# Optimization experiments

Measured on AMD Instinct MI355X. Metric: run time of the kernel, lower is better.

The kernel has to match this reference:

```python
import jax, jax.numpy as jnp
import numpy as np

DT = 0.1
WHEELBASE = 2.8
STATE_DIM = 12


def setup_inputs() -> dict:
    key = jax.random.key(0)
    k1, k2, k3 = jax.random.split(key, 3)
    b, l, h = 512, 64, 80
    x0 = jax.random.normal(k1, (b, STATE_DIM), dtype=jnp.float32)
    controls = jax.random.normal(k2, (b, l, h, 3), dtype=jnp.float32)
    deg = jax.random.uniform(k3, (b, 5), dtype=jnp.float32)
    return {"x0": x0, "controls": controls, "deg": deg}


def reference(x0, controls, deg):
    b, l, h, _ = controls.shape
    # degradation scales, broadcast over the l (candidate) dim: [b, 1]
    steer_scale = jnp.maximum(deg[:, 0:1], 0.05)
    brake_scale = jnp.maximum(deg[:, 1:2], 0.05)
    throttle_scale = jnp.maximum(deg[:, 2:3], 0.05)
    friction = jnp.maximum(deg[:, 4:5], 0.1)

    x_init = jnp.broadcast_to(x0[:, None, :], (b, l, x0.shape[-1]))  # [b,l,12]

    def step(x, u):  # x: [b,l,12], u: [b,l,3]
        delta = steer_scale * jnp.tanh(u[..., 0])
        fb = brake_scale * jax.nn.sigmoid(u[..., 1])
        fx = throttle_scale * jax.nn.sigmoid(u[..., 2])
        px, py, psi, vx, vy = (x[..., 0], x[..., 1], x[..., 2], x[..., 3], x[..., 4])
        speed = jnp.sqrt(vx * vx + vy * vy + 1e-06)
        acc = jnp.minimum(jnp.maximum(2.8 * fx - 6.5 * fb, -7.5 * friction), 3.0)
        speed2 = jnp.maximum(speed + acc * DT, 0.0)
        tan_d = jnp.tan(jnp.clip(delta, -0.75, 0.75))
        raw_yaw = speed2 / WHEELBASE * tan_d
        yaw_lim = jnp.maximum(friction * 9.81 / jnp.maximum(speed2, 2.0), 0.15)
        yaw_rate = jnp.clip(raw_yaw, -1.0, 1.0) * yaw_lim
        beta = jnp.clip(jnp.arctan(0.45 * tan_d), -0.65, 0.65)
        psi2 = psi + yaw_rate * DT
        vx2 = speed2 * jnp.cos(psi2 + beta)
        vy2 = speed2 * jnp.sin(psi2 + beta)
        px2 = px + vx2 * DT
        py2 = py + vy2 * DT
        ax = (vx2 - vx) / DT
        ay = (vy2 - vy) / DT
        x2 = jnp.stack([px2, py2, psi2, vx2, vy2, yaw_rate, ax, ay, beta, delta, fb, fx], -1)
        return x2, x2

    controls_t = jnp.moveaxis(controls, 2, 0)  # [h,b,l,3]
    _, traj = jax.lax.scan(step, x_init, controls_t)  # traj: [h,b,l,12]
    traj = jnp.concatenate([x_init[None], traj], axis=0)  # [h+1,b,l,12]
    return jnp.moveaxis(traj, 0, 2)  # [b,l,h+1,12]
```

## Files before the change

kernel.cpp:

```cpp
#include <hip/hip_runtime.h>
#include <math.h>


#define N_B 512
#define N_L 64
#define N_H 80
#define DT_F 0.1f
#define PITCH_F4 25
#define SPC 8
#define NCH 10

__device__ __forceinline__ float fast_rcp(float x) { return __builtin_amdgcn_rcpf(x); }

__device__ __forceinline__ float fast_tanh(float x) {
    const float e2 = __expf(2.0f * x);
    return (e2 - 1.0f) * fast_rcp(e2 + 1.0f);
}

__device__ __forceinline__ float fast_sigmoid(float x) {
    return fast_rcp(1.0f + __expf(-x));
}

__device__ __forceinline__ float fast_atan_small(float z) {
    const float z2 = z * z;
    float p = 1.0f / 9.0f;
    p = fmaf(p, z2, -1.0f / 7.0f);
    p = fmaf(p, z2, 1.0f / 5.0f);
    p = fmaf(p, z2, -1.0f / 3.0f);
    p = fmaf(p, z2, 1.0f);
    return z * p;
}

struct Ctl { float delta, fb, fx, tan_d, beta, acc; };

__device__ __forceinline__ Ctl make_ctl(float u0, float u1, float u2,
                                        float steer_scale, float brake_scale,
                                        float throttle_scale, float neg_brake_lim) {
    Ctl t;
    t.delta = steer_scale * fast_tanh(u0);
    t.fb = brake_scale    * fast_sigmoid(u1);
    t.fx = throttle_scale * fast_sigmoid(u2);
    const float dc = fminf(fmaxf(t.delta, -0.75f), 0.75f);
    float sd, cd;
    __sincosf(dc, &sd, &cd);
    t.tan_d = sd * fast_rcp(cd);
    t.beta = fminf(fmaxf(fast_atan_small(0.45f * t.tan_d), -0.65f), 0.65f);
    t.acc = fminf(fmaxf(2.8f * t.fx - 6.5f * t.fb, neg_brake_lim), 3.0f);
    return t;
}

__global__ __launch_bounds__(64) void degraded_bicycle_rollout_kernel(
    const float* __restrict__ x0,
    const float* __restrict__ controls,
    const float* __restrict__ deg,
    float* __restrict__ out)
{
    __shared__ float4 lds4[2][N_L * PITCH_F4];

    const int lane = threadIdx.x;
    const int b = blockIdx.x;
    const int tid = b * 64 + lane;

    const float* dg = deg + b * 5;
    const float steer_scale    = fmaxf(dg[0], 0.05f);
    const float brake_scale    = fmaxf(dg[1], 0.05f);
    const float throttle_scale = fmaxf(dg[2], 0.05f);
    const float friction       = fmaxf(dg[4], 0.1f);

    const float4* x0v = reinterpret_cast<const float4*>(x0 + b * 12);
    const float4 xi0 = x0v[0];
    const float4 xi1 = x0v[1];
    const float4 xi2 = x0v[2];

    {
        float4* ov = reinterpret_cast<float4*>(out + (size_t)tid * 972);
        ov[0] = xi0; ov[1] = xi1; ov[2] = xi2;
    }

    float px  = xi0.x;
    float py  = xi0.y;
    float psi = xi0.z;
    float vx  = xi0.w;
    float vy  = xi1.x;

    const float4* uc = reinterpret_cast<const float4*>(controls + (size_t)tid * 240);

    const float neg_brake_lim = -7.5f * friction;
    const float yaw_num = friction * 9.81f;
    const float inv_wheelbase = 1.0f / 2.8f;

    const size_t out_b = (size_t)b * 62208 + 12;

#define FLUSH_SLICE(FBUF, FC, I0, I1)                                             \
    {                                                                             \
        const size_t obase = out_b + (size_t)(FC) * (SPC * 12);                   \
        _Pragma("unroll")                                                         \
        for (int i = (I0); i < (I1); ++i) {                                       \
            const unsigned flat = i * 64 + lane;                                  \
            const unsigned l = flat / 24u;                                        \
            const unsigned q = flat - l * 24u;                                    \
            const float4 v = lds4[FBUF][l * PITCH_F4 + q];                        \
            *reinterpret_cast<float4*>(out + obase + (size_t)l * 972 + q * 4) = v;\
        }                                                                         \
    }

    float4 c0 = uc[0];
    float4 c1 = uc[1];
    float4 c2 = uc[2];

    for (int c = 0; c < NCH; ++c) {
        const int cur = c & 1;
        float4* lrow = &lds4[cur][lane * PITCH_F4];

        #pragma unroll
        for (int gg = 0; gg < 2; ++gg) {
            const int g = c * 2 + gg;
            float4 n0 = c0, n1 = c1, n2 = c2;
            if (g < 19) {
                n0 = uc[(g + 1) * 3 + 0];
                n1 = uc[(g + 1) * 3 + 1];
                n2 = uc[(g + 1) * 3 + 2];
            }

            const Ctl tA = make_ctl(c0.x, c0.y, c0.z, steer_scale, brake_scale, throttle_scale, neg_brake_lim);
            const Ctl tB = make_ctl(c0.w, c1.x, c1.y, steer_scale, brake_scale, throttle_scale, neg_brake_lim);
            const Ctl tC = make_ctl(c1.z, c1.w, c2.x, steer_scale, brake_scale, throttle_scale, neg_brake_lim);
            const Ctl tD = make_ctl(c2.y, c2.z, c2.w, steer_scale, brake_scale, throttle_scale, neg_brake_lim);

#define ROLL_STEP(T, RR)                                                          \
            {                                                                     \
                const float speed  = __builtin_amdgcn_sqrtf(fmaf(vx, vx, fmaf(vy, vy, 1e-6f))); \
                const float speed2 = fmaxf(fmaf((T).acc, DT_F, speed), 0.0f);     \
                const float raw_yaw = speed2 * inv_wheelbase * (T).tan_d;         \
                const float yaw_lim = fmaxf(yaw_num * fast_rcp(fmaxf(speed2, 2.0f)), 0.15f); \
                const float yaw_rate = fminf(fmaxf(raw_yaw, -1.0f), 1.0f) * yaw_lim; \
                const float psi2 = fmaf(yaw_rate, DT_F, psi);                     \
                float s_, c_;                                                     \
                __sincosf(psi2 + (T).beta, &s_, &c_);                             \
                const float vx2 = speed2 * c_;                                    \
                const float vy2 = speed2 * s_;                                    \
                const float px2 = fmaf(vx2, DT_F, px);                            \
                const float py2 = fmaf(vy2, DT_F, py);                            \
                const float ax = (vx2 - vx) * 10.0f;                              \
                const float ay = (vy2 - vy) * 10.0f;                              \
                lrow[(RR) * 3 + 0] = make_float4(px2, py2, psi2, vx2);            \
                lrow[(RR) * 3 + 1] = make_float4(vy2, yaw_rate, ax, ay);          \
                lrow[(RR) * 3 + 2] = make_float4((T).beta, (T).delta, (T).fb, (T).fx); \
                px = px2; py = py2; psi = psi2; vx = vx2; vy = vy2;               \
            }

            ROLL_STEP(tA, gg * 4 + 0)
            ROLL_STEP(tB, gg * 4 + 1)
            ROLL_STEP(tC, gg * 4 + 2)
            ROLL_STEP(tD, gg * 4 + 3)
#undef ROLL_STEP

            c0 = n0; c1 = n1; c2 = n2;

            if (c > 0) {
                if (gg == 0) FLUSH_SLICE(cur ^ 1, c - 1, 0, 12)
                else         FLUSH_SLICE(cur ^ 1, c - 1, 12, 24)
            }
        }
    }

    FLUSH_SLICE((NCH - 1) & 1, NCH - 1, 0, 24)
#undef FLUSH_SLICE
}

extern "C" void kernel_launch(void* const* d_in, const int* in_sizes, int n_in,
                              void* d_out, int out_size, void* d_ws, size_t ws_size,
                              hipStream_t stream) {
    (void)in_sizes; (void)n_in; (void)d_ws; (void)ws_size; (void)out_size;
    const float* x0       = (const float*)d_in[0];
    const float* controls = (const float*)d_in[1];
    const float* deg      = (const float*)d_in[2];
    float* out            = (float*)d_out;

    dim3 grid(N_B), block(64);
    hipLaunchKernelGGL(degraded_bicycle_rollout_kernel, grid, block, 0, stream,
                       x0, controls, deg, out);
}
```

Measured before the change: 35.43 us.

## Split block into compute wave and store wave with LDS double-buffer handoff

Blocks grow to two waves. Wave 0 runs the sequential rollout and writes chunks into a double-buffered LDS area, while wave 1 copies the previous chunk from LDS to global memory, with __syncthreads separating the chunks. The intent is to take the global store traffic off the latency-bound compute wave so stores and compute overlap. The cost is a block-wide barrier per chunk and twice the threads per block. Wave 1 also takes over the initial-state writes, using a coalesced layout.

```diff
diff --git a/kernel.cpp b/kernel.cpp
--- a/kernel.cpp
+++ b/kernel.cpp
@@ -49,7 +49,7 @@
     return t;
 }
 
-__global__ __launch_bounds__(64) void degraded_bicycle_rollout_kernel(
+__global__ __launch_bounds__(128) void degraded_bicycle_rollout_kernel(
     const float* __restrict__ x0,
     const float* __restrict__ controls,
     const float* __restrict__ deg,
@@ -57,43 +57,15 @@
 {
     __shared__ float4 lds4[2][N_L * PITCH_F4];
 
-    const int lane = threadIdx.x;
+    const int lane = threadIdx.x & 63;
+    const int wave = threadIdx.x >> 6;
     const int b = blockIdx.x;
-    const int tid = b * 64 + lane;
 
-    const float* dg = deg + b * 5;
-    const float steer_scale    = fmaxf(dg[0], 0.05f);
-    const float brake_scale    = fmaxf(dg[1], 0.05f);
-    const float throttle_scale = fmaxf(dg[2], 0.05f);
-    const float friction       = fmaxf(dg[4], 0.1f);
-
-    const float4* x0v = reinterpret_cast<const float4*>(x0 + b * 12);
-    const float4 xi0 = x0v[0];
-    const float4 xi1 = x0v[1];
-    const float4 xi2 = x0v[2];
-
-    {
-        float4* ov = reinterpret_cast<float4*>(out + (size_t)tid * 972);
-        ov[0] = xi0; ov[1] = xi1; ov[2] = xi2;
-    }
-
-    float px  = xi0.x;
-    float py  = xi0.y;
-    float psi = xi0.z;
-    float vx  = xi0.w;
-    float vy  = xi1.x;
-
-    const float4* uc = reinterpret_cast<const float4*>(controls + (size_t)tid * 240);
-
-    const float neg_brake_lim = -7.5f * friction;
-    const float yaw_num = friction * 9.81f;
-    const float inv_wheelbase = 1.0f / 2.8f;
-
-    const size_t out_b = (size_t)b * 62208 + 12;
+    const size_t out_b = (size_t)b * 62208;
 
 #define FLUSH_SLICE(FBUF, FC, I0, I1)                                             \
     {                                                                             \
-        const size_t obase = out_b + (size_t)(FC) * (SPC * 12);                   \
+        const size_t obase = out_b + 12 + (size_t)(FC) * (SPC * 12);              \
         _Pragma("unroll")                                                         \
         for (int i = (I0); i < (I1); ++i) {                                       \
             const unsigned flat = i * 64 + lane;                                  \
@@ -104,67 +76,105 @@
         }                                                                         \
     }
 
-    float4 c0 = uc[0];
-    float4 c1 = uc[1];
-    float4 c2 = uc[2];
+    if (wave == 0) {
+        const float* dg = deg + b * 5;
+        const float steer_scale    = fmaxf(dg[0], 0.05f);
+        const float brake_scale    = fmaxf(dg[1], 0.05f);
+        const float throttle_scale = fmaxf(dg[2], 0.05f);
+        const float friction       = fmaxf(dg[4], 0.1f);
 
-    for (int c = 0; c < NCH; ++c) {
-        const int cur = c & 1;
-        float4* lrow = &lds4[cur][lane * PITCH_F4];
+        const float4* x0v = reinterpret_cast<const float4*>(x0 + b * 12);
+        const float4 xi0 = x0v[0];
+        const float4 xi1 = x0v[1];
 
-        #pragma unroll
-        for (int gg = 0; gg < 2; ++gg) {
-            const int g = c * 2 + gg;
-            float4 n0 = c0, n1 = c1, n2 = c2;
-            if (g < 19) {
-                n0 = uc[(g + 1) * 3 + 0];
-                n1 = uc[(g + 1) * 3 + 1];
-                n2 = uc[(g + 1) * 3 + 2];
-            }
+        float px  = xi0.x;
+        float py  = xi0.y;
+        float psi = xi0.z;
+        float vx  = xi0.w;
+        float vy  = xi1.x;
 
-            const Ctl tA = make_ctl(c0.x, c0.y, c0.z, steer_scale, brake_scale, throttle_scale, neg_brake_lim);
-            const Ctl tB = make_ctl(c0.w, c1.x, c1.y, steer_scale, brake_scale, throttle_scale, neg_brake_lim);
-            const Ctl tC = make_ctl(c1.z, c1.w, c2.x, steer_scale, brake_scale, throttle_scale, neg_brake_lim);
-            const Ctl tD = make_ctl(c2.y, c2.z, c2.w, steer_scale, brake_scale, throttle_scale, neg_brake_lim);
+        const int tid = b * 64 + lane;
+        const float4* uc = reinterpret_cast<const float4*>(controls + (size_t)tid * 240);
+
+        const float neg_brake_lim = -7.5f * friction;
+        const float yaw_num = friction * 9.81f;
+        const float inv_wheelbase = 1.0f / 2.8f;
+
+        float4 c0 = uc[0];
+        float4 c1 = uc[1];
+        float4 c2 = uc[2];
+
+        for (int c = 0; c < NCH; ++c) {
+            float4* lrow = &lds4[c & 1][lane * PITCH_F4];
+
+            #pragma unroll
+            for (int gg = 0; gg < 2; ++gg) {
+                const int g = c * 2 + gg;
+                float4 n0 = c0, n1 = c1, n2 = c2;
+                if (g < 19) {
+                    n0 = uc[(g + 1) * 3 + 0];
+                    n1 = uc[(g + 1) * 3 + 1];
+                    n2 = uc[(g + 1) * 3 + 2];
+                }
+
+                const Ctl tA = make_ctl(c0.x, c0.y, c0.z, steer_scale, brake_scale, throttle_scale, neg_brake_lim);
+                const Ctl tB = make_ctl(c0.w, c1.x, c1.y, steer_scale, brake_scale, throttle_scale, neg_brake_lim);
+                const Ctl tC = make_ctl(c1.z, c1.w, c2.x, steer_scale, brake_scale, throttle_scale, neg_brake_lim);
+                const Ctl tD = make_ctl(c2.y, c2.z, c2.w, steer_scale, brake_scale, throttle_scale, neg_brake_lim);
 
 #define ROLL_STEP(T, RR)                                                          \
-            {                                                                     \
-                const float speed  = __builtin_amdgcn_sqrtf(fmaf(vx, vx, fmaf(vy, vy, 1e-6f))); \
-                const float speed2 = fmaxf(fmaf((T).acc, DT_F, speed), 0.0f);     \
-                const float raw_yaw = speed2 * inv_wheelbase * (T).tan_d;         \
-                const float yaw_lim = fmaxf(yaw_num * fast_rcp(fmaxf(speed2, 2.0f)), 0.15f); \
-                const float yaw_rate = fminf(fmaxf(raw_yaw, -1.0f), 1.0f) * yaw_lim; \
-                const float psi2 = fmaf(yaw_rate, DT_F, psi);                     \
-                float s_, c_;                                                     \
-                __sincosf(psi2 + (T).beta, &s_, &c_);                             \
-                const float vx2 = speed2 * c_;                                    \
-                const float vy2 = speed2 * s_;                                    \
-                const float px2 = fmaf(vx2, DT_F, px);                            \
-                const float py2 = fmaf(vy2, DT_F, py);                            \
-                const float ax = (vx2 - vx) * 10.0f;                              \
-                const float ay = (vy2 - vy) * 10.0f;                              \
-                lrow[(RR) * 3 + 0] = make_float4(px2, py2, psi2, vx2);            \
-                lrow[(RR) * 3 + 1] = make_float4(vy2, yaw_rate, ax, ay);          \
-                lrow[(RR) * 3 + 2] = make_float4((T).beta, (T).delta, (T).fb, (T).fx); \
-                px = px2; py = py2; psi = psi2; vx = vx2; vy = vy2;               \
-            }
+                {                                                                 \
+                    const float speed  = __builtin_amdgcn_sqrtf(fmaf(vx, vx, fmaf(vy, vy, 1e-6f))); \
+                    const float speed2 = fmaxf(fmaf((T).acc, DT_F, speed), 0.0f); \
+                    const float raw_yaw = speed2 * inv_wheelbase * (T).tan_d;     \
+                    const float yaw_lim = fmaxf(yaw_num * fast_rcp(fmaxf(speed2, 2.0f)), 0.15f); \
+                    const float yaw_rate = fminf(fmaxf(raw_yaw, -1.0f), 1.0f) * yaw_lim; \
+                    const float psi2 = fmaf(yaw_rate, DT_F, psi);                 \
+                    float s_, c_;                                                 \
+                    __sincosf(psi2 + (T).beta, &s_, &c_);                         \
+                    const float vx2 = speed2 * c_;                                \
+                    const float vy2 = speed2 * s_;                                \
+                    const float px2 = fmaf(vx2, DT_F, px);                        \
+                    const float py2 = fmaf(vy2, DT_F, py);                        \
+                    const float ax = (vx2 - vx) * 10.0f;                          \
+                    const float ay = (vy2 - vy) * 10.0f;                          \
+                    lrow[(RR) * 3 + 0] = make_float4(px2, py2, psi2, vx2);        \
+                    lrow[(RR) * 3 + 1] = make_float4(vy2, yaw_rate, ax, ay);      \
+                    lrow[(RR) * 3 + 2] = make_float4((T).beta, (T).delta, (T).fb, (T).fx); \
+                    px = px2; py = py2; psi = psi2; vx = vx2; vy = vy2;           \
+                }
 
-            ROLL_STEP(tA, gg * 4 + 0)
-            ROLL_STEP(tB, gg * 4 + 1)
-            ROLL_STEP(tC, gg * 4 + 2)
-            ROLL_STEP(tD, gg * 4 + 3)
+                ROLL_STEP(tA, gg * 4 + 0)
+                ROLL_STEP(tB, gg * 4 + 1)
+                ROLL_STEP(tC, gg * 4 + 2)
+                ROLL_STEP(tD, gg * 4 + 3)
 #undef ROLL_STEP
 
-            c0 = n0; c1 = n1; c2 = n2;
-
-            if (c > 0) {
-                if (gg == 0) FLUSH_SLICE(cur ^ 1, c - 1, 0, 12)
-                else         FLUSH_SLICE(cur ^ 1, c - 1, 12, 24)
+                c0 = n0; c1 = n1; c2 = n2;
+            }
+            __syncthreads();
+        }
+    } else {
+        {
+            const float4* x0v = reinterpret_cast<const float4*>(x0 + b * 12);
+            const float4 xq0 = x0v[0];
+            const float4 xq1 = x0v[1];
+            const float4 xq2 = x0v[2];
+            #pragma unroll
+            for (int i = 0; i < 3; ++i) {
+                const unsigned flat = i * 64 + lane;
+                const unsigned l = flat / 3u;
+                const unsigned q = flat - l * 3u;
+                const float4 v = (q == 0) ? xq0 : (q == 1) ? xq1 : xq2;
+                *reinterpret_cast<float4*>(out + out_b + (size_t)l * 972 + q * 4) = v;
             }
         }
+        for (int c = 0; c < NCH; ++c) {
+            if (c > 0) FLUSH_SLICE((c - 1) & 1, c - 1, 0, 24)
+            __syncthreads();
+        }
+        FLUSH_SLICE((NCH - 1) & 1, NCH - 1, 0, 24)
     }
-
-    FLUSH_SLICE((NCH - 1) & 1, NCH - 1, 0, 24)
 #undef FLUSH_SLICE
 }
 
@@ -177,7 +187,7 @@
     const float* deg      = (const float*)d_in[2];
     float* out            = (float*)d_out;
 
-    dim3 grid(N_B), block(64);
+    dim3 grid(N_B), block(128);
     hipLaunchKernelGGL(degraded_bicycle_rollout_kernel, grid, block, 0, stream,
                        x0, controls, deg, out);
 }
```

Measured after the change: 35.25 us. No clear change (-0.5%).
